# Kernel optimization log

Hardware: AMD Instinct MI355X
Metric: run time of the kernel (lower is better)

Reference implementation:

```python
import jax, jax.numpy as jnp
import numpy as np
import math

EMB = 512
HEADS = 8
FM = 56
WS = 7


def _relative_position_index(ws):
    coords = np.stack(np.meshgrid(np.arange(ws), np.arange(ws), indexing='ij')).reshape(2, -1)
    rel = coords[:, :, None] - coords[:, None, :]            # [2, ws^2, ws^2]
    rel = rel.transpose(1, 2, 0)                              # [ws^2, ws^2, 2]
    rel = rel + np.abs(rel.min())                             # shift to >= 0 (adds ws-1)
    rel[:, :, 0] = rel[:, :, 0] * (2 * ws - 1)
    return rel.sum(-1)                                        # [ws^2, ws^2] int

REL_IDX = jnp.asarray(_relative_position_index(WS))


def setup_inputs() -> dict:
    key = jax.random.key(0)
    ks = jax.random.split(key, 8)
    B, L, E = 16, FM * FM, EMB
    scale = 0.02
    return {
        'x': jax.random.normal(ks[0], (B, L, E), dtype=jnp.float32),
        'q_w': jax.random.normal(ks[1], (E, E), dtype=jnp.float32) * scale,
        'q_b': jax.random.normal(ks[2], (E,), dtype=jnp.float32) * scale,
        'k_w': jax.random.normal(ks[3], (E, E), dtype=jnp.float32) * scale,
        'k_b': jax.random.normal(ks[4], (E,), dtype=jnp.float32) * scale,
        'v_w': jax.random.normal(ks[5], (E, E), dtype=jnp.float32) * scale,
        'v_b': jax.random.normal(ks[6], (E,), dtype=jnp.float32) * scale,
        'bias_table': jax.random.normal(ks[7], ((2 * WS - 1) ** 2, HEADS), dtype=jnp.float32) * scale,
    }


def reference(x, q_w, q_b, k_w, k_b, v_w, v_b, bias_table):
    B, L, E = x.shape
    nh, d, ws = HEADS, E // HEADS, WS
    n = ws * ws
    # Faithful to the torch code: reshape (NOT channels-last transpose), then window partition
    xr = x.reshape(B, E, FM, FM)
    w = xr.reshape(B, FM // ws, ws, FM // ws, ws, E)
    w = jnp.transpose(w, (0, 1, 3, 2, 4, 5)).reshape(B, -1, ws, ws, E)  # [B, nW, ws, ws, E]
    nW = w.shape[1]
    # Linear projections (torch Linear: x @ W.T + b)
    q = (w @ q_w.T + q_b).reshape(B, nW, nh, n, d)
    k = (w @ k_w.T + k_b).reshape(B, nW, nh, n, d)
    v = (w @ v_w.T + v_b).reshape(B, nW, nh, n, d)
    # Relative position bias: [nh, n, n]
    bias = bias_table[REL_IDX.reshape(-1)].reshape(n, n, nh).transpose(2, 0, 1)
    scores = jnp.einsum('bwhqd,bwhkd->bwhqk', q, k) / math.sqrt(d)
    scores = scores + bias[None, None]
    attn = jax.nn.softmax(scores, axis=-1)
    out = jnp.einsum('bwhqk,bwhkd->bwhqd', attn, v)
    return out.reshape(B, L, E)
```

## Files before the change

kernel.cpp:

```cpp
#include <hip/hip_runtime.h>

typedef __attribute__((ext_vector_type(8))) short short8;
typedef __attribute__((ext_vector_type(4))) short short4v;
typedef __attribute__((ext_vector_type(4))) float float4v;
typedef __attribute__((ext_vector_type(8))) __bf16 bf16x8;

#define LDS_PQ 57344
#define LDS_PK 107520
#define LDS_TOTAL 157696

__device__ __forceinline__ unsigned short f2bf(float f) {
  unsigned u = __float_as_uint(f);
  u += 0x7FFFu + ((u >> 16) & 1u);
  return (unsigned short)(u >> 16);
}

__device__ __forceinline__ int pswz(int s) { return ((s ^ (s >> 3)) & 7) << 4; }

__global__ void wconv_kernel(const float* __restrict__ qw, const float* __restrict__ kw,
                             const float* __restrict__ vw, short* __restrict__ out) {
  int idx = blockIdx.x * 256 + threadIdx.x;
  int g = idx >> 15;
  int rem = idx & 32767;
  int lane = rem & 63;
  int n01 = (rem >> 6) & 1;
  int w   = (rem >> 7) & 15;
  int kk  = rem >> 11;
  int o  = w * 32 + n01 * 16 + (lane & 15);
  int k0 = kk * 32 + (lane >> 4) * 8;
  const float* src = (g == 0) ? qw : (g == 1) ? kw : vw;
  const float* p = src + o * 512 + k0;
  float4v v0 = *(const float4v*)(p);
  float4v v1 = *(const float4v*)(p + 4);
  short8 o8;
  o8[0] = (short)f2bf(v0.x); o8[1] = (short)f2bf(v0.y);
  o8[2] = (short)f2bf(v0.z); o8[3] = (short)f2bf(v0.w);
  o8[4] = (short)f2bf(v1.x); o8[5] = (short)f2bf(v1.y);
  o8[6] = (short)f2bf(v1.z); o8[7] = (short)f2bf(v1.w);
  *(short8*)(out + idx * 8) = o8;
}

__global__ void bexp_kernel(const float* __restrict__ btab, float* __restrict__ bexp) {
  int idx = blockIdx.x * 256 + threadIdx.x;
  float v = 0.f;
  if (idx < 21952) {
    int h = idx / 2744;
    int rem = idx - h * 2744;
    int i = rem / 56;
    int j = rem - i * 56;
    if (j < 49) {
      int yi = (i * 37) >> 8, xi = i - yi * 7;
      int yj = (j * 37) >> 8, xj = j - yj * 7;
      int t = (yi - yj + 6) * 13 + (xi - xj + 6);
      v = btab[t * 8 + h];
    }
  }
  bexp[idx] = v;
}

__global__ __launch_bounds__(1024, 4) void wattn_kernel(
    const float* __restrict__ x, const short* __restrict__ wcvt,
    const float* __restrict__ qb, const float* __restrict__ kb, const float* __restrict__ vb,
    const float* __restrict__ bexp, float* __restrict__ out) {
  __shared__ __align__(16) char sm[LDS_TOTAL];
  const int tid  = threadIdx.x;
  const int lane = tid & 63;
  const int wave = tid >> 6;
  const int bwi  = blockIdx.x;
  const int bb   = bwi >> 6, wi = bwi & 63;
  const int l15  = lane & 15;
  const int l4   = lane >> 4;
  const int ig   = l4 * 4;

  {
    const float* xb = x + (size_t)bb * (3136 * 512);
    const int whi = (wi >> 3) * 7, wlo = (wi & 7) * 7;
    for (int idx = tid; idx < 49 * 128; idx += 1024) {
      int t = idx >> 7, c4 = idx & 127;
      int yt = (t * 37) >> 8, xt = t - yt * 7;
      int l = (whi + yt) * 56 + wlo + xt;
      float4v v = *(const float4v*)(xb + l * 512 + c4 * 4);
      short4v o;
      o.x = (short)f2bf(v.x); o.y = (short)f2bf(v.y);
      o.z = (short)f2bf(v.z); o.w = (short)f2bf(v.w);
      int byte = t * 1024 + c4 * 8;
      *(short4v*)(sm + (byte ^ ((t & 7) << 4))) = o;
    }
  }
  __syncthreads();

  const int wcol = wave * 32;
  const int ckof = l4 * 16;

  int xbase[4], xsw[4];
#pragma unroll
  for (int mt = 0; mt < 4; ++mt) {
    int row = mt * 16 + l15;
    xbase[mt] = row * 1024;
    xsw[mt]   = (row & 7) << 4;
  }

  const short* wgb0 = wcvt + wave * 1024 + lane * 8;

#define LDWP(P, OFF) __builtin_bit_cast(bf16x8, *(const short8*)((P) + (OFF)))
#define LDX(MT, C) __builtin_bit_cast(bf16x8, *(const short8*)(sm + xbase[MT] + ((C) ^ xsw[MT])))

  {
    const short* wq = wgb0;
    const short* wk = wgb0 + 262144;
    float4v aq[2][4], ak[2][4];
#pragma unroll
    for (int nt = 0; nt < 2; ++nt)
#pragma unroll
      for (int mt = 0; mt < 4; ++mt) { aq[nt][mt] = (float4v)0.f; ak[nt][mt] = (float4v)0.f; }

    bf16x8 uq0 = LDWP(wq, 0), uq1 = LDWP(wq, 512);
    bf16x8 uk0 = LDWP(wk, 0), uk1 = LDWP(wk, 512);

#pragma unroll 1
    for (int kk = 0; kk < 16; ++kk) {
      const int nko = ((kk + 1) & 15) * 16384;
      bf16x8 nq0 = LDWP(wq, nko), nq1 = LDWP(wq, nko + 512);
      bf16x8 nk0 = LDWP(wk, nko), nk1 = LDWP(wk, nko + 512);
      const int c_ = kk * 64 + ckof;
      bf16x8 x0 = LDX(0, c_), x1 = LDX(1, c_), x2 = LDX(2, c_), x3 = LDX(3, c_);
      __builtin_amdgcn_s_setprio(1);
      aq[0][0] = __builtin_amdgcn_mfma_f32_16x16x32_bf16(uq0, x0, aq[0][0], 0, 0, 0);
      aq[1][0] = __builtin_amdgcn_mfma_f32_16x16x32_bf16(uq1, x0, aq[1][0], 0, 0, 0);
      ak[0][0] = __builtin_amdgcn_mfma_f32_16x16x32_bf16(uk0, x0, ak[0][0], 0, 0, 0);
      ak[1][0] = __builtin_amdgcn_mfma_f32_16x16x32_bf16(uk1, x0, ak[1][0], 0, 0, 0);
      aq[0][1] = __builtin_amdgcn_mfma_f32_16x16x32_bf16(uq0, x1, aq[0][1], 0, 0, 0);
      aq[1][1] = __builtin_amdgcn_mfma_f32_16x16x32_bf16(uq1, x1, aq[1][1], 0, 0, 0);
      ak[0][1] = __builtin_amdgcn_mfma_f32_16x16x32_bf16(uk0, x1, ak[0][1], 0, 0, 0);
      ak[1][1] = __builtin_amdgcn_mfma_f32_16x16x32_bf16(uk1, x1, ak[1][1], 0, 0, 0);
      aq[0][2] = __builtin_amdgcn_mfma_f32_16x16x32_bf16(uq0, x2, aq[0][2], 0, 0, 0);
      aq[1][2] = __builtin_amdgcn_mfma_f32_16x16x32_bf16(uq1, x2, aq[1][2], 0, 0, 0);
      ak[0][2] = __builtin_amdgcn_mfma_f32_16x16x32_bf16(uk0, x2, ak[0][2], 0, 0, 0);
      ak[1][2] = __builtin_amdgcn_mfma_f32_16x16x32_bf16(uk1, x2, ak[1][2], 0, 0, 0);
      aq[0][3] = __builtin_amdgcn_mfma_f32_16x16x32_bf16(uq0, x3, aq[0][3], 0, 0, 0);
      aq[1][3] = __builtin_amdgcn_mfma_f32_16x16x32_bf16(uq1, x3, aq[1][3], 0, 0, 0);
      ak[0][3] = __builtin_amdgcn_mfma_f32_16x16x32_bf16(uk0, x3, ak[0][3], 0, 0, 0);
      ak[1][3] = __builtin_amdgcn_mfma_f32_16x16x32_bf16(uk1, x3, ak[1][3], 0, 0, 0);
      __builtin_amdgcn_s_setprio(0);
      uq0 = nq0; uq1 = nq1; uk0 = nk0; uk1 = nk1;
    }

#pragma unroll
    for (int nt = 0; nt < 2; ++nt) {
      int o0 = wcol + nt * 16 + ig;
      float4v bq = *(const float4v*)(qb + o0);
      float4v bk = *(const float4v*)(kb + o0);
      int dd0 = o0 & 63, sg = o0 >> 6;
#pragma unroll
      for (int mt = 0; mt < 4; ++mt) {
        int t = mt * 16 + l15;
        if (t < 49) {
          int s = t * 8 + sg;
          int addr = (s * 128 + dd0 * 2) ^ pswz(s);
          short4v pq, pk;
#pragma unroll
          for (int r = 0; r < 4; ++r) {
            pq[r] = (short)f2bf((aq[nt][mt][r] + bq[r]) * 0.125f);
            pk[r] = (short)f2bf(ak[nt][mt][r] + bk[r]);
          }
          *(short4v*)(sm + LDS_PQ + addr) = pq;
          *(short4v*)(sm + LDS_PK + addr) = pk;
        }
      }
    }
  }

  {
    const short* wgb = wgb0 + 2 * 262144;
    float4v acc[2][4];
#pragma unroll
    for (int nt = 0; nt < 2; ++nt)
#pragma unroll
      for (int mt = 0; mt < 4; ++mt) acc[nt][mt] = (float4v)0.f;

    bf16x8 wa0 = LDWP(wgb, 0),     wa1 = LDWP(wgb, 512);
    bf16x8 wb0 = LDWP(wgb, 16384), wb1 = LDWP(wgb, 16384 + 512);
    bf16x8 wc0, wc1, wd0, wd1;

#define GEMM_PHASE(KIDX, W0, W1)                                                          \
    do {                                                                                  \
      const int c_ = (KIDX) * 64 + ckof;                                                  \
      bf16x8 x0_ = LDX(0, c_), x1_ = LDX(1, c_), x2_ = LDX(2, c_), x3_ = LDX(3, c_);      \
      __builtin_amdgcn_s_setprio(1);                                                      \
      acc[0][0] = __builtin_amdgcn_mfma_f32_16x16x32_bf16(W0, x0_, acc[0][0], 0, 0, 0);   \
      acc[1][0] = __builtin_amdgcn_mfma_f32_16x16x32_bf16(W1, x0_, acc[1][0], 0, 0, 0);   \
      acc[0][1] = __builtin_amdgcn_mfma_f32_16x16x32_bf16(W0, x1_, acc[0][1], 0, 0, 0);   \
      acc[1][1] = __builtin_amdgcn_mfma_f32_16x16x32_bf16(W1, x1_, acc[1][1], 0, 0, 0);   \
      acc[0][2] = __builtin_amdgcn_mfma_f32_16x16x32_bf16(W0, x2_, acc[0][2], 0, 0, 0);   \
      acc[1][2] = __builtin_amdgcn_mfma_f32_16x16x32_bf16(W1, x2_, acc[1][2], 0, 0, 0);   \
      acc[0][3] = __builtin_amdgcn_mfma_f32_16x16x32_bf16(W0, x3_, acc[0][3], 0, 0, 0);   \
      acc[1][3] = __builtin_amdgcn_mfma_f32_16x16x32_bf16(W1, x3_, acc[1][3], 0, 0, 0);   \
      __builtin_amdgcn_s_setprio(0);                                                      \
    } while (0)

#pragma unroll 1
    for (int kk = 0; kk < 16; kk += 4) {
      wc0 = LDWP(wgb, ((kk + 2) & 15) * 16384); wc1 = LDWP(wgb, ((kk + 2) & 15) * 16384 + 512);
      GEMM_PHASE(kk, wa0, wa1);
      wd0 = LDWP(wgb, ((kk + 3) & 15) * 16384); wd1 = LDWP(wgb, ((kk + 3) & 15) * 16384 + 512);
      GEMM_PHASE(kk + 1, wb0, wb1);
      wa0 = LDWP(wgb, ((kk + 4) & 15) * 16384); wa1 = LDWP(wgb, ((kk + 4) & 15) * 16384 + 512);
      GEMM_PHASE(kk + 2, wc0, wc1);
      wb0 = LDWP(wgb, ((kk + 5) & 15) * 16384); wb1 = LDWP(wgb, ((kk + 5) & 15) * 16384 + 512);
      GEMM_PHASE(kk + 3, wd0, wd1);
    }
#undef GEMM_PHASE

    __syncthreads();
#pragma unroll
    for (int nt = 0; nt < 2; ++nt) {
      int o0 = wcol + nt * 16 + ig;
      float4v bv = *(const float4v*)(vb + o0);
      int dd0 = o0 & 63, sg = o0 >> 6;
#pragma unroll
      for (int mt = 0; mt < 4; ++mt) {
        int t = mt * 16 + l15;
        if (t < 49) {
          int s = t * 8 + sg;
          int h2 = (s * 1339) >> 16;
          int colb = h2 * 112 + (s - h2 * 49) * 2;
#pragma unroll
          for (int r = 0; r < 4; ++r) {
            int dd = dd0 + r;
            *(unsigned short*)(sm + ((dd * 896 + colb) ^ ((dd & 7) << 4))) =
                f2bf(acc[nt][mt][r] + bv[r]);
          }
        }
      }
    }
    if (tid < 512) {
      int h2 = tid >> 6, dd = tid & 63;
      int rowb = dd * 896 + h2 * 112;
      int swz = (dd & 7) << 4;
#pragma unroll
      for (int q = 49; q < 56; ++q)
        *(unsigned short*)(sm + ((rowb + q * 2) ^ swz)) = 0;
    }
  }

  const int h  = wave & 7;
  const int mh = wave >> 3;

  float4v sc[4][2];
#pragma unroll
  for (int jt = 0; jt < 4; ++jt)
#pragma unroll
    for (int it = 0; it < 2; ++it) sc[jt][it] = (float4v)0.f;

#pragma unroll
  for (int ks = 0; ks < 2; ++ks) {
    const int dd = ks * 32 + l4 * 8;
    bf16x8 kf[4], qf[2];
#pragma unroll
    for (int jt = 0; jt < 4; ++jt) {
      int s = h * 49 + jt * 16 + l15;
      int flat = s * 128 + dd * 2;
      kf[jt] = __builtin_bit_cast(bf16x8, *(const short8*)(sm + LDS_PK + (flat ^ pswz(s))));
    }
#pragma unroll
    for (int it = 0; it < 2; ++it) {
      int s = h * 49 + (mh * 2 + it) * 16 + l15;
      int flat = s * 128 + dd * 2;
      qf[it] = __builtin_bit_cast(bf16x8, *(const short8*)(sm + LDS_PQ + (flat ^ pswz(s))));
    }
    __builtin_amdgcn_s_setprio(1);
#pragma unroll
    for (int jt = 0; jt < 4; ++jt)
#pragma unroll
      for (int it = 0; it < 2; ++it)
        sc[jt][it] = __builtin_amdgcn_mfma_f32_16x16x32_bf16(kf[jt], qf[it], sc[jt][it], 0, 0, 0);
    __builtin_amdgcn_s_setprio(0);
  }

  const float* bx = bexp + h * 2744;
#pragma unroll
  for (int it = 0; it < 2; ++it) {
    int i = (mh * 2 + it) * 16 + l15;
    const float* bi = bx + ((i > 48) ? 48 : i) * 56 + ig;
    float mx = -1e30f;
#pragma unroll
    for (int jt = 0; jt < 4; ++jt) {
      float4v b4 = *(const float4v*)(bi + jt * 16);
#pragma unroll
      for (int r = 0; r < 4; ++r) {
        int j = jt * 16 + ig + r;
        float v = (i < 49 && j < 49) ? sc[jt][it][r] + b4[r] : -1e30f;
        sc[jt][it][r] = v;
        mx = fmaxf(mx, v);
      }
    }
    mx = fmaxf(mx, __shfl_xor(mx, 16));
    mx = fmaxf(mx, __shfl_xor(mx, 32));
    float ssum = 0.f;
#pragma unroll
    for (int jt = 0; jt < 4; ++jt)
#pragma unroll
      for (int r = 0; r < 4; ++r) {
        float e = __expf(sc[jt][it][r] - mx);
        sc[jt][it][r] = e;
        ssum += e;
      }
    ssum += __shfl_xor(ssum, 16);
    ssum += __shfl_xor(ssum, 32);
    float inv = 1.f / ssum;
#pragma unroll
    for (int jt = 0; jt < 4; ++jt)
#pragma unroll
      for (int r = 0; r < 4; ++r) sc[jt][it][r] *= inv;
  }

#pragma unroll
  for (int it = 0; it < 2; ++it) {
    int i = (mh * 2 + it) * 16 + l15;
    if (i < 49) {
      int s = h * 49 + i;
      int rowb = s * 128;
      int swz = pswz(s);
#pragma unroll
      for (int jt = 0; jt < 4; ++jt) {
        short4v pk;
#pragma unroll
        for (int r = 0; r < 4; ++r) pk[r] = (short)f2bf(sc[jt][it][r]);
        *(short4v*)(sm + LDS_PQ + ((rowb + jt * 32 + ig * 2) ^ swz)) = pk;
      }
    }
  }

  __syncthreads();

  float4v oacc[4][2];
#pragma unroll
  for (int dt = 0; dt < 4; ++dt)
#pragma unroll
    for (int tt = 0; tt < 2; ++tt) oacc[dt][tt] = (float4v)0.f;

#pragma unroll
  for (int ks = 0; ks < 2; ++ks) {
    const int tp0 = ks * 32 + l4 * 8;
    bf16x8 vf[4], af[2];
#pragma unroll
    for (int dt = 0; dt < 4; ++dt) {
      int dd = dt * 16 + l15;
      vf[dt] = __builtin_bit_cast(bf16x8,
          *(const short8*)(sm + ((dd * 896 + h * 112 + tp0 * 2) ^ ((dd & 7) << 4))));
    }
#pragma unroll
    for (int tt = 0; tt < 2; ++tt) {
      int t = (mh * 2 + tt) * 16 + l15;
      int tr = (t > 48) ? 48 : t;
      int s = h * 49 + tr;
      af[tt] = __builtin_bit_cast(bf16x8,
          *(const short8*)(sm + LDS_PQ + ((s * 128 + tp0 * 2) ^ pswz(s))));
    }
    __builtin_amdgcn_s_setprio(1);
#pragma unroll
    for (int dt = 0; dt < 4; ++dt)
#pragma unroll
      for (int tt = 0; tt < 2; ++tt)
        oacc[dt][tt] = __builtin_amdgcn_mfma_f32_16x16x32_bf16(vf[dt], af[tt], oacc[dt][tt], 0, 0, 0);
    __builtin_amdgcn_s_setprio(0);
  }

  float* op = out + (size_t)bwi * 25088 + h * 3136;
#pragma unroll
  for (int tt = 0; tt < 2; ++tt) {
    int t = (mh * 2 + tt) * 16 + l15;
    if (t < 49) {
#pragma unroll
      for (int dt = 0; dt < 4; ++dt)
        *(float4v*)(op + t * 64 + dt * 16 + ig) = oacc[dt][tt];
    }
  }
#undef LDWP
#undef LDX
}

extern "C" void kernel_launch(void* const* d_in, const int* in_sizes, int n_in,
                              void* d_out, int out_size, void* d_ws, size_t ws_size,
                              hipStream_t stream) {
  const float* x    = (const float*)d_in[0];
  const float* q_w  = (const float*)d_in[1];
  const float* q_b  = (const float*)d_in[2];
  const float* k_w  = (const float*)d_in[3];
  const float* k_b  = (const float*)d_in[4];
  const float* v_w  = (const float*)d_in[5];
  const float* v_b  = (const float*)d_in[6];
  const float* btab = (const float*)d_in[7];
  short* wcvt = (short*)d_ws;
  float* bexp = (float*)((char*)d_ws + 3 * 262144 * 2);

  hipLaunchKernelGGL(wconv_kernel, dim3(384), dim3(256), 0, stream, q_w, k_w, v_w, wcvt);
  hipLaunchKernelGGL(bexp_kernel, dim3(86), dim3(256), 0, stream, btab, bexp);
  hipLaunchKernelGGL(wattn_kernel, dim3(1024), dim3(1024), 0, stream,
                     x, wcvt, q_b, k_b, v_b, bexp, (float*)d_out);
}
```

Before: 149.4 us.

## Make attention kernel persistent over windows, fold q scale into weights, use packed bf16 converts

The main kernel now launches 256 blocks that each loop over four windows, instead of one block per window for 1024 blocks. A barrier at the top of each iteration protects shared-memory reuse. The 1/sqrt(d) query scale moves into the weight-conversion pre-kernel and the bias, and f32-to-bf16 rounding now uses the hardware v_cvt_pk_bf16_f32 instruction instead of integer bit manipulation. The goal is less block launch and tail overhead and fewer ALU ops, at the risk of lower parallelism, since 256 blocks with roughly 154 KB of LDS each may leave some CUs idle, with no overlap of load and compute across iterations.

Measured after the change: 241.3 us. +61.5%, slower.

```diff
diff --git a/kernel.cpp b/kernel.cpp
--- a/kernel.cpp
+++ b/kernel.cpp
@@ -3,6 +3,7 @@
 typedef __attribute__((ext_vector_type(8))) short short8;
 typedef __attribute__((ext_vector_type(4))) short short4v;
 typedef __attribute__((ext_vector_type(4))) float float4v;
+typedef __attribute__((ext_vector_type(2))) unsigned int uint2v;
 typedef __attribute__((ext_vector_type(8))) __bf16 bf16x8;
 
 #define LDS_PQ 57344
@@ -13,6 +14,12 @@
   unsigned u = __float_as_uint(f);
   u += 0x7FFFu + ((u >> 16) & 1u);
   return (unsigned short)(u >> 16);
+}
+
+__device__ __forceinline__ unsigned cvtpk(float lo, float hi) {
+  unsigned r;
+  asm("v_cvt_pk_bf16_f32 %0, %1, %2" : "=v"(r) : "v"(lo), "v"(hi));
+  return r;
 }
 
 __device__ __forceinline__ int pswz(int s) { return ((s ^ (s >> 3)) & 7) << 4; }
@@ -29,14 +36,15 @@
   int o  = w * 32 + n01 * 16 + (lane & 15);
   int k0 = kk * 32 + (lane >> 4) * 8;
   const float* src = (g == 0) ? qw : (g == 1) ? kw : vw;
+  const float sc = (g == 0) ? 0.125f : 1.0f;
   const float* p = src + o * 512 + k0;
   float4v v0 = *(const float4v*)(p);
   float4v v1 = *(const float4v*)(p + 4);
   short8 o8;
-  o8[0] = (short)f2bf(v0.x); o8[1] = (short)f2bf(v0.y);
-  o8[2] = (short)f2bf(v0.z); o8[3] = (short)f2bf(v0.w);
-  o8[4] = (short)f2bf(v1.x); o8[5] = (short)f2bf(v1.y);
-  o8[6] = (short)f2bf(v1.z); o8[7] = (short)f2bf(v1.w);
+  o8[0] = (short)f2bf(v0.x * sc); o8[1] = (short)f2bf(v0.y * sc);
+  o8[2] = (short)f2bf(v0.z * sc); o8[3] = (short)f2bf(v0.w * sc);
+  o8[4] = (short)f2bf(v1.x * sc); o8[5] = (short)f2bf(v1.y * sc);
+  o8[6] = (short)f2bf(v1.z * sc); o8[7] = (short)f2bf(v1.w * sc);
   *(short8*)(out + idx * 8) = o8;
 }
 
@@ -66,31 +74,13 @@
   const int tid  = threadIdx.x;
   const int lane = tid & 63;
   const int wave = tid >> 6;
-  const int bwi  = blockIdx.x;
-  const int bb   = bwi >> 6, wi = bwi & 63;
   const int l15  = lane & 15;
   const int l4   = lane >> 4;
   const int ig   = l4 * 4;
-
-  {
-    const float* xb = x + (size_t)bb * (3136 * 512);
-    const int whi = (wi >> 3) * 7, wlo = (wi & 7) * 7;
-    for (int idx = tid; idx < 49 * 128; idx += 1024) {
-      int t = idx >> 7, c4 = idx & 127;
-      int yt = (t * 37) >> 8, xt = t - yt * 7;
-      int l = (whi + yt) * 56 + wlo + xt;
-      float4v v = *(const float4v*)(xb + l * 512 + c4 * 4);
-      short4v o;
-      o.x = (short)f2bf(v.x); o.y = (short)f2bf(v.y);
-      o.z = (short)f2bf(v.z); o.w = (short)f2bf(v.w);
-      int byte = t * 1024 + c4 * 8;
-      *(short4v*)(sm + (byte ^ ((t & 7) << 4))) = o;
-    }
-  }
-  __syncthreads();
-
   const int wcol = wave * 32;
   const int ckof = l4 * 16;
+  const int h    = wave & 7;
+  const int mh   = wave >> 3;
 
   int xbase[4], xsw[4];
 #pragma unroll
@@ -105,275 +95,297 @@
 #define LDWP(P, OFF) __builtin_bit_cast(bf16x8, *(const short8*)((P) + (OFF)))
 #define LDX(MT, C) __builtin_bit_cast(bf16x8, *(const short8*)(sm + xbase[MT] + ((C) ^ xsw[MT])))
 
-  {
-    const short* wq = wgb0;
-    const short* wk = wgb0 + 262144;
-    float4v aq[2][4], ak[2][4];
-#pragma unroll
-    for (int nt = 0; nt < 2; ++nt)
-#pragma unroll
-      for (int mt = 0; mt < 4; ++mt) { aq[nt][mt] = (float4v)0.f; ak[nt][mt] = (float4v)0.f; }
-
-    bf16x8 uq0 = LDWP(wq, 0), uq1 = LDWP(wq, 512);
-    bf16x8 uk0 = LDWP(wk, 0), uk1 = LDWP(wk, 512);
-
 #pragma unroll 1
-    for (int kk = 0; kk < 16; ++kk) {
-      const int nko = ((kk + 1) & 15) * 16384;
-      bf16x8 nq0 = LDWP(wq, nko), nq1 = LDWP(wq, nko + 512);
-      bf16x8 nk0 = LDWP(wk, nko), nk1 = LDWP(wk, nko + 512);
-      const int c_ = kk * 64 + ckof;
-      bf16x8 x0 = LDX(0, c_), x1 = LDX(1, c_), x2 = LDX(2, c_), x3 = LDX(3, c_);
-      __builtin_amdgcn_s_setprio(1);
-      aq[0][0] = __builtin_amdgcn_mfma_f32_16x16x32_bf16(uq0, x0, aq[0][0], 0, 0, 0);
-      aq[1][0] = __builtin_amdgcn_mfma_f32_16x16x32_bf16(uq1, x0, aq[1][0], 0, 0, 0);
-      ak[0][0] = __builtin_amdgcn_mfma_f32_16x16x32_bf16(uk0, x0, ak[0][0], 0, 0, 0);
-      ak[1][0] = __builtin_amdgcn_mfma_f32_16x16x32_bf16(uk1, x0, ak[1][0], 0, 0, 0);
-      aq[0][1] = __builtin_amdgcn_mfma_f32_16x16x32_bf16(uq0, x1, aq[0][1], 0, 0, 0);
-      aq[1][1] = __builtin_amdgcn_mfma_f32_16x16x32_bf16(uq1, x1, aq[1][1], 0, 0, 0);
-      ak[0][1] = __builtin_amdgcn_mfma_f32_16x16x32_bf16(uk0, x1, ak[0][1], 0, 0, 0);
-      ak[1][1] = __builtin_amdgcn_mfma_f32_16x16x32_bf16(uk1, x1, ak[1][1], 0, 0, 0);
-      aq[0][2] = __builtin_amdgcn_mfma_f32_16x16x32_bf16(uq0, x2, aq[0][2], 0, 0, 0);
-      aq[1][2] = __builtin_amdgcn_mfma_f32_16x16x32_bf16(uq1, x2, aq[1][2], 0, 0, 0);
-      ak[0][2] = __builtin_amdgcn_mfma_f32_16x16x32_bf16(uk0, x2, ak[0][2], 0, 0, 0);
-      ak[1][2] = __builtin_amdgcn_mfma_f32_16x16x32_bf16(uk1, x2, ak[1][2], 0, 0, 0);
-      aq[0][3] = __builtin_amdgcn_mfma_f32_16x16x32_bf16(uq0, x3, aq[0][3], 0, 0, 0);
-      aq[1][3] = __builtin_amdgcn_mfma_f32_16x16x32_bf16(uq1, x3, aq[1][3], 0, 0, 0);
-      ak[0][3] = __builtin_amdgcn_mfma_f32_16x16x32_bf16(uk0, x3, ak[0][3], 0, 0, 0);
-      ak[1][3] = __builtin_amdgcn_mfma_f32_16x16x32_bf16(uk1, x3, ak[1][3], 0, 0, 0);
-      __builtin_amdgcn_s_setprio(0);
-      uq0 = nq0; uq1 = nq1; uk0 = nk0; uk1 = nk1;
-    }
-
-#pragma unroll
-    for (int nt = 0; nt < 2; ++nt) {
-      int o0 = wcol + nt * 16 + ig;
-      float4v bq = *(const float4v*)(qb + o0);
-      float4v bk = *(const float4v*)(kb + o0);
-      int dd0 = o0 & 63, sg = o0 >> 6;
-#pragma unroll
-      for (int mt = 0; mt < 4; ++mt) {
-        int t = mt * 16 + l15;
-        if (t < 49) {
-          int s = t * 8 + sg;
-          int addr = (s * 128 + dd0 * 2) ^ pswz(s);
-          short4v pq, pk;
-#pragma unroll
-          for (int r = 0; r < 4; ++r) {
-            pq[r] = (short)f2bf((aq[nt][mt][r] + bq[r]) * 0.125f);
-            pk[r] = (short)f2bf(ak[nt][mt][r] + bk[r]);
-          }
-          *(short4v*)(sm + LDS_PQ + addr) = pq;
-          *(short4v*)(sm + LDS_PK + addr) = pk;
-        }
-      }
-    }
-  }
-
-  {
-    const short* wgb = wgb0 + 2 * 262144;
-    float4v acc[2][4];
-#pragma unroll
-    for (int nt = 0; nt < 2; ++nt)
-#pragma unroll
-      for (int mt = 0; mt < 4; ++mt) acc[nt][mt] = (float4v)0.f;
-
-    bf16x8 wa0 = LDWP(wgb, 0),     wa1 = LDWP(wgb, 512);
-    bf16x8 wb0 = LDWP(wgb, 16384), wb1 = LDWP(wgb, 16384 + 512);
-    bf16x8 wc0, wc1, wd0, wd1;
-
-#define GEMM_PHASE(KIDX, W0, W1)                                                          \
-    do {                                                                                  \
-      const int c_ = (KIDX) * 64 + ckof;                                                  \
-      bf16x8 x0_ = LDX(0, c_), x1_ = LDX(1, c_), x2_ = LDX(2, c_), x3_ = LDX(3, c_);      \
-      __builtin_amdgcn_s_setprio(1);                                                      \
-      acc[0][0] = __builtin_amdgcn_mfma_f32_16x16x32_bf16(W0, x0_, acc[0][0], 0, 0, 0);   \
-      acc[1][0] = __builtin_amdgcn_mfma_f32_16x16x32_bf16(W1, x0_, acc[1][0], 0, 0, 0);   \
-      acc[0][1] = __builtin_amdgcn_mfma_f32_16x16x32_bf16(W0, x1_, acc[0][1], 0, 0, 0);   \
-      acc[1][1] = __builtin_amdgcn_mfma_f32_16x16x32_bf16(W1, x1_, acc[1][1], 0, 0, 0);   \
-      acc[0][2] = __builtin_amdgcn_mfma_f32_16x16x32_bf16(W0, x2_, acc[0][2], 0, 0, 0);   \
-      acc[1][2] = __builtin_amdgcn_mfma_f32_16x16x32_bf16(W1, x2_, acc[1][2], 0, 0, 0);   \
-      acc[0][3] = __builtin_amdgcn_mfma_f32_16x16x32_bf16(W0, x3_, acc[0][3], 0, 0, 0);   \
-      acc[1][3] = __builtin_amdgcn_mfma_f32_16x16x32_bf16(W1, x3_, acc[1][3], 0, 0, 0);   \
-      __builtin_amdgcn_s_setprio(0);                                                      \
-    } while (0)
+  for (int bwi = blockIdx.x; bwi < 1024; bwi += 256) {
+    const int bb = bwi >> 6, wi = bwi & 63;
+
+    __syncthreads();
+
+    {
+      const float* xb = x + (size_t)bb * (3136 * 512);
+      const int whi = (wi >> 3) * 7, wlo = (wi & 7) * 7;
+      for (int idx = tid; idx < 49 * 128; idx += 1024) {
+        int t = idx >> 7, c4 = idx & 127;
+        int yt = (t * 37) >> 8, xt = t - yt * 7;
+        int l = (whi + yt) * 56 + wlo + xt;
+        float4v v = *(const float4v*)(xb + l * 512 + c4 * 4);
+        uint2v o;
+        o.x = cvtpk(v.x, v.y);
+        o.y = cvtpk(v.z, v.w);
+        int byte = t * 1024 + c4 * 8;
+        *(uint2v*)(sm + (byte ^ ((t & 7) << 4))) = o;
+      }
+    }
+    __syncthreads();
+
+    {
+      const short* wq = wgb0;
+      const short* wk = wgb0 + 262144;
+      float4v aq[2][4], ak[2][4];
+#pragma unroll
+      for (int nt = 0; nt < 2; ++nt)
+#pragma unroll
+        for (int mt = 0; mt < 4; ++mt) { aq[nt][mt] = (float4v)0.f; ak[nt][mt] = (float4v)0.f; }
+
+      bf16x8 uq0 = LDWP(wq, 0), uq1 = LDWP(wq, 512);
+      bf16x8 uk0 = LDWP(wk, 0), uk1 = LDWP(wk, 512);
 
 #pragma unroll 1
-    for (int kk = 0; kk < 16; kk += 4) {
-      wc0 = LDWP(wgb, ((kk + 2) & 15) * 16384); wc1 = LDWP(wgb, ((kk + 2) & 15) * 16384 + 512);
-      GEMM_PHASE(kk, wa0, wa1);
-      wd0 = LDWP(wgb, ((kk + 3) & 15) * 16384); wd1 = LDWP(wgb, ((kk + 3) & 15) * 16384 + 512);
-      GEMM_PHASE(kk + 1, wb0, wb1);
-      wa0 = LDWP(wgb, ((kk + 4) & 15) * 16384); wa1 = LDWP(wgb, ((kk + 4) & 15) * 16384 + 512);
-      GEMM_PHASE(kk + 2, wc0, wc1);
-      wb0 = LDWP(wgb, ((kk + 5) & 15) * 16384); wb1 = LDWP(wgb, ((kk + 5) & 15) * 16384 + 512);
-      GEMM_PHASE(kk + 3, wd0, wd1);
-    }
-#undef GEMM_PHASE
-
-    __syncthreads();
-#pragma unroll
-    for (int nt = 0; nt < 2; ++nt) {
-      int o0 = wcol + nt * 16 + ig;
-      float4v bv = *(const float4v*)(vb + o0);
-      int dd0 = o0 & 63, sg = o0 >> 6;
-#pragma unroll
-      for (int mt = 0; mt < 4; ++mt) {
-        int t = mt * 16 + l15;
-        if (t < 49) {
-          int s = t * 8 + sg;
-          int h2 = (s * 1339) >> 16;
-          int colb = h2 * 112 + (s - h2 * 49) * 2;
-#pragma unroll
-          for (int r = 0; r < 4; ++r) {
-            int dd = dd0 + r;
-            *(unsigned short*)(sm + ((dd * 896 + colb) ^ ((dd & 7) << 4))) =
-                f2bf(acc[nt][mt][r] + bv[r]);
+      for (int kk = 0; kk < 16; ++kk) {
+        const int nko = ((kk + 1) & 15) * 16384;
+        bf16x8 nq0 = LDWP(wq, nko), nq1 = LDWP(wq, nko + 512);
+        bf16x8 nk0 = LDWP(wk, nko), nk1 = LDWP(wk, nko + 512);
+        const int c_ = kk * 64 + ckof;
+        bf16x8 x0 = LDX(0, c_), x1 = LDX(1, c_), x2 = LDX(2, c_), x3 = LDX(3, c_);
+        __builtin_amdgcn_s_setprio(1);
+        aq[0][0] = __builtin_amdgcn_mfma_f32_16x16x32_bf16(uq0, x0, aq[0][0], 0, 0, 0);
+        aq[1][0] = __builtin_amdgcn_mfma_f32_16x16x32_bf16(uq1, x0, aq[1][0], 0, 0, 0);
+        ak[0][0] = __builtin_amdgcn_mfma_f32_16x16x32_bf16(uk0, x0, ak[0][0], 0, 0, 0);
+        ak[1][0] = __builtin_amdgcn_mfma_f32_16x16x32_bf16(uk1, x0, ak[1][0], 0, 0, 0);
+        aq[0][1] = __builtin_amdgcn_mfma_f32_16x16x32_bf16(uq0, x1, aq[0][1], 0, 0, 0);
+        aq[1][1] = __builtin_amdgcn_mfma_f32_16x16x32_bf16(uq1, x1, aq[1][1], 0, 0, 0);
+        ak[0][1] = __builtin_amdgcn_mfma_f32_16x16x32_bf16(uk0, x1, ak[0][1], 0, 0, 0);
+        ak[1][1] = __builtin_amdgcn_mfma_f32_16x16x32_bf16(uk1, x1, ak[1][1], 0, 0, 0);
+        aq[0][2] = __builtin_amdgcn_mfma_f32_16x16x32_bf16(uq0, x2, aq[0][2], 0, 0, 0);
+        aq[1][2] = __builtin_amdgcn_mfma_f32_16x16x32_bf16(uq1, x2, aq[1][2], 0, 0, 0);
+        ak[0][2] = __builtin_amdgcn_mfma_f32_16x16x32_bf16(uk0, x2, ak[0][2], 0, 0, 0);
+        ak[1][2] = __builtin_amdgcn_mfma_f32_16x16x32_bf16(uk1, x2, ak[1][2], 0, 0, 0);
+        aq[0][3] = __builtin_amdgcn_mfma_f32_16x16x32_bf16(uq0, x3, aq[0][3], 0, 0, 0);
+        aq[1][3] = __builtin_amdgcn_mfma_f32_16x16x32_bf16(uq1, x3, aq[1][3], 0, 0, 0);
+        ak[0][3] = __builtin_amdgcn_mfma_f32_16x16x32_bf16(uk0, x3, ak[0][3], 0, 0, 0);
+        ak[1][3] = __builtin_amdgcn_mfma_f32_16x16x32_bf16(uk1, x3, ak[1][3], 0, 0, 0);
+        __builtin_amdgcn_s_setprio(0);
+        uq0 = nq0; uq1 = nq1; uk0 = nk0; uk1 = nk1;
+      }
+
+#pragma unroll
+      for (int nt = 0; nt < 2; ++nt) {
+        int o0 = wcol + nt * 16 + ig;
+        float4v bq = *(const float4v*)(qb + o0);
+        float4v bk = *(const float4v*)(kb + o0);
+#pragma unroll
+        for (int r = 0; r < 4; ++r) bq[r] *= 0.125f;
+        int dd0 = o0 & 63, sg = o0 >> 6;
+#pragma unroll
+        for (int mt = 0; mt < 4; ++mt) {
+          int t = mt * 16 + l15;
+          if (t < 49) {
+            int s = t * 8 + sg;
+            int addr = (s * 128 + dd0 * 2) ^ pswz(s);
+            uint2v pq, pk;
+            pq.x = cvtpk(aq[nt][mt][0] + bq[0], aq[nt][mt][1] + bq[1]);
+            pq.y = cvtpk(aq[nt][mt][2] + bq[2], aq[nt][mt][3] + bq[3]);
+            pk.x = cvtpk(ak[nt][mt][0] + bk[0], ak[nt][mt][1] + bk[1]);
+            pk.y = cvtpk(ak[nt][mt][2] + bk[2], ak[nt][mt][3] + bk[3]);
+            *(uint2v*)(sm + LDS_PQ + addr) = pq;
+            *(uint2v*)(sm + LDS_PK + addr) = pk;
           }
         }
       }
     }
-    if (tid < 512) {
-      int h2 = tid >> 6, dd = tid & 63;
-      int rowb = dd * 896 + h2 * 112;
-      int swz = (dd & 7) << 4;
-#pragma unroll
-      for (int q = 49; q < 56; ++q)
-        *(unsigned short*)(sm + ((rowb + q * 2) ^ swz)) = 0;
-    }
-  }
-
-  const int h  = wave & 7;
-  const int mh = wave >> 3;
-
-  float4v sc[4][2];
-#pragma unroll
-  for (int jt = 0; jt < 4; ++jt)
-#pragma unroll
-    for (int it = 0; it < 2; ++it) sc[jt][it] = (float4v)0.f;
-
-#pragma unroll
-  for (int ks = 0; ks < 2; ++ks) {
-    const int dd = ks * 32 + l4 * 8;
-    bf16x8 kf[4], qf[2];
-#pragma unroll
-    for (int jt = 0; jt < 4; ++jt) {
-      int s = h * 49 + jt * 16 + l15;
-      int flat = s * 128 + dd * 2;
-      kf[jt] = __builtin_bit_cast(bf16x8, *(const short8*)(sm + LDS_PK + (flat ^ pswz(s))));
-    }
+
+    {
+      const short* wgb = wgb0 + 2 * 262144;
+      float4v acc[2][4];
+#pragma unroll
+      for (int nt = 0; nt < 2; ++nt)
+#pragma unroll
+        for (int mt = 0; mt < 4; ++mt) acc[nt][mt] = (float4v)0.f;
+
+      bf16x8 wa0 = LDWP(wgb, 0),     wa1 = LDWP(wgb, 512);
+      bf16x8 wb0 = LDWP(wgb, 16384), wb1 = LDWP(wgb, 16384 + 512);
+      bf16x8 wc0, wc1, wd0, wd1;
+
+#define GEMM_PHASE(KIDX, W0, W1)                                                          \
+      do {                                                                                \
+        const int c_ = (KIDX) * 64 + ckof;                                                \
+        bf16x8 x0_ = LDX(0, c_), x1_ = LDX(1, c_), x2_ = LDX(2, c_), x3_ = LDX(3, c_);    \
+        __builtin_amdgcn_s_setprio(1);                                                    \
+        acc[0][0] = __builtin_amdgcn_mfma_f32_16x16x32_bf16(W0, x0_, acc[0][0], 0, 0, 0); \
+        acc[1][0] = __builtin_amdgcn_mfma_f32_16x16x32_bf16(W1, x0_, acc[1][0], 0, 0, 0); \
+        acc[0][1] = __builtin_amdgcn_mfma_f32_16x16x32_bf16(W0, x1_, acc[0][1], 0, 0, 0); \
+        acc[1][1] = __builtin_amdgcn_mfma_f32_16x16x32_bf16(W1, x1_, acc[1][1], 0, 0, 0); \
+        acc[0][2] = __builtin_amdgcn_mfma_f32_16x16x32_bf16(W0, x2_, acc[0][2], 0, 0, 0); \
+        acc[1][2] = __builtin_amdgcn_mfma_f32_16x16x32_bf16(W1, x2_, acc[1][2], 0, 0, 0); \
+        acc[0][3] = __builtin_amdgcn_mfma_f32_16x16x32_bf16(W0, x3_, acc[0][3], 0, 0, 0); \
+        acc[1][3] = __builtin_amdgcn_mfma_f32_16x16x32_bf16(W1, x3_, acc[1][3], 0, 0, 0); \
+        __builtin_amdgcn_s_setprio(0);                                                    \
+      } while (0)
+
+#pragma unroll 1
+      for (int kk = 0; kk < 16; kk += 4) {
+        wc0 = LDWP(wgb, ((kk + 2) & 15) * 16384); wc1 = LDWP(wgb, ((kk + 2) & 15) * 16384 + 512);
+        GEMM_PHASE(kk, wa0, wa1);
+        wd0 = LDWP(wgb, ((kk + 3) & 15) * 16384); wd1 = LDWP(wgb, ((kk + 3) & 15) * 16384 + 512);
+        GEMM_PHASE(kk + 1, wb0, wb1);
+        wa0 = LDWP(wgb, ((kk + 4) & 15) * 16384); wa1 = LDWP(wgb, ((kk + 4) & 15) * 16384 + 512);
+        GEMM_PHASE(kk + 2, wc0, wc1);
+        wb0 = LDWP(wgb, ((kk + 5) & 15) * 16384); wb1 = LDWP(wgb, ((kk + 5) & 15) * 16384 + 512);
+        GEMM_PHASE(kk + 3, wd0, wd1);
+      }
+#undef GEMM_PHASE
+
+      __syncthreads();
+#pragma unroll
+      for (int nt = 0; nt < 2; ++nt) {
+        int o0 = wcol + nt * 16 + ig;
+        float4v bv = *(const float4v*)(vb + o0);
+        int dd0 = o0 & 63, sg = o0 >> 6;
+#pragma unroll
+        for (int mt = 0; mt < 4; ++mt) {
+          int t = mt * 16 + l15;
+          if (t < 49) {
+            int s = t * 8 + sg;
+            int h2 = (s * 1339) >> 16;
+            int colb = h2 * 112 + (s - h2 * 49) * 2;
+#pragma unroll
+            for (int r = 0; r < 4; ++r) {
+              int dd = dd0 + r;
+              *(unsigned short*)(sm + ((dd * 896 + colb) ^ ((dd & 7) << 4))) =
+                  f2bf(acc[nt][mt][r] + bv[r]);
+            }
+          }
+        }
+      }
+      if (tid < 512) {
+        int h2 = tid >> 6, dd = tid & 63;
+        int rowb = dd * 896 + h2 * 112;
+        int swz = (dd & 7) << 4;
+#pragma unroll
+        for (int q = 49; q < 56; ++q)
+          *(unsigned short*)(sm + ((rowb + q * 2) ^ swz)) = 0;
+      }
+    }
+
+    float4v sc[4][2];
+#pragma unroll
+    for (int jt = 0; jt < 4; ++jt)
+#pragma unroll
+      for (int it = 0; it < 2; ++it) sc[jt][it] = (float4v)0.f;
+
+#pragma unroll
+    for (int ks = 0; ks < 2; ++ks) {
+      const int dd = ks * 32 + l4 * 8;
+      bf16x8 kf[4], qf[2];
+#pragma unroll
+      for (int jt = 0; jt < 4; ++jt) {
+        int s = h * 49 + jt * 16 + l15;
+        int flat = s * 128 + dd * 2;
+        kf[jt] = __builtin_bit_cast(bf16x8, *(const short8*)(sm + LDS_PK + (flat ^ pswz(s))));
+      }
+#pragma unroll
+      for (int it = 0; it < 2; ++it) {
+        int s = h * 49 + (mh * 2 + it) * 16 + l15;
+        int flat = s * 128 + dd * 2;
+        qf[it] = __builtin_bit_cast(bf16x8, *(const short8*)(sm + LDS_PQ + (flat ^ pswz(s))));
+      }
+      __builtin_amdgcn_s_setprio(1);
+#pragma unroll
+      for (int jt = 0; jt < 4; ++jt)
+#pragma unroll
+        for (int it = 0; it < 2; ++it)
+          sc[jt][it] = __builtin_amdgcn_mfma_f32_16x16x32_bf16(kf[jt], qf[it], sc[jt][it], 0, 0, 0);
+      __builtin_amdgcn_s_setprio(0);
+    }
+
+    const float* bx = bexp + h * 2744;
 #pragma unroll
     for (int it = 0; it < 2; ++it) {
-      int s = h * 49 + (mh * 2 + it) * 16 + l15;
-      int flat = s * 128 + dd * 2;
-      qf[it] = __builtin_bit_cast(bf16x8, *(const short8*)(sm + LDS_PQ + (flat ^ pswz(s))));
-    }
-    __builtin_amdgcn_s_setprio(1);
-#pragma unroll
-    for (int jt = 0; jt < 4; ++jt)
-#pragma unroll
-      for (int it = 0; it < 2; ++it)
-        sc[jt][it] = __builtin_amdgcn_mfma_f32_16x16x32_bf16(kf[jt], qf[it], sc[jt][it], 0, 0, 0);
-    __builtin_amdgcn_s_setprio(0);
-  }
-
-  const float* bx = bexp + h * 2744;
-#pragma unroll
-  for (int it = 0; it < 2; ++it) {
-    int i = (mh * 2 + it) * 16 + l15;
-    const float* bi = bx + ((i > 48) ? 48 : i) * 56 + ig;
-    float mx = -1e30f;
-#pragma unroll
-    for (int jt = 0; jt < 4; ++jt) {
-      float4v b4 = *(const float4v*)(bi + jt * 16);
-#pragma unroll
-      for (int r = 0; r < 4; ++r) {
-        int j = jt * 16 + ig + r;
-        float v = (i < 49 && j < 49) ? sc[jt][it][r] + b4[r] : -1e30f;
-        sc[jt][it][r] = v;
-        mx = fmaxf(mx, v);
-      }
-    }
-    mx = fmaxf(mx, __shfl_xor(mx, 16));
-    mx = fmaxf(mx, __shfl_xor(mx, 32));
-    float ssum = 0.f;
-#pragma unroll
-    for (int jt = 0; jt < 4; ++jt)
-#pragma unroll
-      for (int r = 0; r < 4; ++r) {
-        float e = __expf(sc[jt][it][r] - mx);
-        sc[jt][it][r] = e;
-        ssum += e;
-      }
-    ssum += __shfl_xor(ssum, 16);
-    ssum += __shfl_xor(ssum, 32);
-    float inv = 1.f / ssum;
-#pragma unroll
-    for (int jt = 0; jt < 4; ++jt)
-#pragma unroll
-      for (int r = 0; r < 4; ++r) sc[jt][it][r] *= inv;
-  }
-
-#pragma unroll
-  for (int it = 0; it < 2; ++it) {
-    int i = (mh * 2 + it) * 16 + l15;
-    if (i < 49) {
-      int s = h * 49 + i;
-      int rowb = s * 128;
-      int swz = pswz(s);
+      int i = (mh * 2 + it) * 16 + l15;
+      const float* bi = bx + ((i > 48) ? 48 : i) * 56 + ig;
+      float mx = -1e30f;
 #pragma unroll
       for (int jt = 0; jt < 4; ++jt) {
-        short4v pk;
-#pragma unroll
-        for (int r = 0; r < 4; ++r) pk[r] = (short)f2bf(sc[jt][it][r]);
-        *(short4v*)(sm + LDS_PQ + ((rowb + jt * 32 + ig * 2) ^ swz)) = pk;
-      }
-    }
-  }
-
-  __syncthreads();
-
-  float4v oacc[4][2];
-#pragma unroll
-  for (int dt = 0; dt < 4; ++dt)
-#pragma unroll
-    for (int tt = 0; tt < 2; ++tt) oacc[dt][tt] = (float4v)0.f;
-
-#pragma unroll
-  for (int ks = 0; ks < 2; ++ks) {
-    const int tp0 = ks * 32 + l4 * 8;
-    bf16x8 vf[4], af[2];
-#pragma unroll
-    for (int dt = 0; dt < 4; ++dt) {
-      int dd = dt * 16 + l15;
-      vf[dt] = __builtin_bit_cast(bf16x8,
-          *(const short8*)(sm + ((dd * 896 + h * 112 + tp0 * 2) ^ ((dd & 7) << 4))));
-    }
+        float4v b4 = *(const float4v*)(bi + jt * 16);
+#pragma unroll
+        for (int r = 0; r < 4; ++r) {
+          int j = jt * 16 + ig + r;
+          float v = (i < 49 && j < 49) ? sc[jt][it][r] + b4[r] : -1e30f;
+          sc[jt][it][r] = v;
+          mx = fmaxf(mx, v);
+        }
+      }
+      mx = fmaxf(mx, __shfl_xor(mx, 16));
+      mx = fmaxf(mx, __shfl_xor(mx, 32));
+      float ssum = 0.f;
+#pragma unroll
+      for (int jt = 0; jt < 4; ++jt)
+#pragma unroll
+        for (int r = 0; r < 4; ++r) {
+          float e = __expf(sc[jt][it][r] - mx);
+          sc[jt][it][r] = e;
+          ssum += e;
+        }
+      ssum += __shfl_xor(ssum, 16);
+      ssum += __shfl_xor(ssum, 32);
+      float inv = 1.f / ssum;
+#pragma unroll
+      for (int jt = 0; jt < 4; ++jt)
+#pragma unroll
+        for (int r = 0; r < 4; ++r) sc[jt][it][r] *= inv;
+    }
+
+#pragma unroll
+    for (int it = 0; it < 2; ++it) {
+      int i = (mh * 2 + it) * 16 + l15;
+      if (i < 49) {
+        int s = h * 49 + i;
+        int rowb = s * 128;
+        int swz = pswz(s);
+#pragma unroll
+        for (int jt = 0; jt < 4; ++jt) {
+          uint2v pk2;
+          pk2.x = cvtpk(sc[jt][it][0], sc[jt][it][1]);
+          pk2.y = cvtpk(sc[jt][it][2], sc[jt][it][3]);
+          *(uint2v*)(sm + LDS_PQ + ((rowb + jt * 32 + ig * 2) ^ swz)) = pk2;
+        }
+      }
+    }
+
+    __syncthreads();
+
+    float4v oacc[4][2];
+#pragma unroll
+    for (int dt = 0; dt < 4; ++dt)
+#pragma unroll
+      for (int tt = 0; tt < 2; ++tt) oacc[dt][tt] = (float4v)0.f;
+
+#pragma unroll
+    for (int ks = 0; ks < 2; ++ks) {
+      const int tp0 = ks * 32 + l4 * 8;
+      bf16x8 vf[4], af[2];
+#pragma unroll
+      for (int dt = 0; dt < 4; ++dt) {
+        int dd = dt * 16 + l15;
+        vf[dt] = __builtin_bit_cast(bf16x8,
+            *(const short8*)(sm + ((dd * 896 + h * 112 + tp0 * 2) ^ ((dd & 7) << 4))));
+      }
+#pragma unroll
+      for (int tt = 0; tt < 2; ++tt) {
+        int t = (mh * 2 + tt) * 16 + l15;
+        int tr = (t > 48) ? 48 : t;
+        int s = h * 49 + tr;
+        af[tt] = __builtin_bit_cast(bf16x8,
+            *(const short8*)(sm + LDS_PQ + ((s * 128 + tp0 * 2) ^ pswz(s))));
+      }
+      __builtin_amdgcn_s_setprio(1);
+#pragma unroll
+      for (int dt = 0; dt < 4; ++dt)
+#pragma unroll
+        for (int tt = 0; tt < 2; ++tt)
+          oacc[dt][tt] = __builtin_amdgcn_mfma_f32_16x16x32_bf16(vf[dt], af[tt], oacc[dt][tt], 0, 0, 0);
+      __builtin_amdgcn_s_setprio(0);
+    }
+
+    float* op = out + (size_t)bwi * 25088 + h * 3136;
 #pragma unroll
     for (int tt = 0; tt < 2; ++tt) {
       int t = (mh * 2 + tt) * 16 + l15;
-      int tr = (t > 48) ? 48 : t;
-      int s = h * 49 + tr;
-      af[tt] = __builtin_bit_cast(bf16x8,
-          *(const short8*)(sm + LDS_PQ + ((s * 128 + tp0 * 2) ^ pswz(s))));
-    }
-    __builtin_amdgcn_s_setprio(1);
-#pragma unroll
-    for (int dt = 0; dt < 4; ++dt)
-#pragma unroll
-      for (int tt = 0; tt < 2; ++tt)
-        oacc[dt][tt] = __builtin_amdgcn_mfma_f32_16x16x32_bf16(vf[dt], af[tt], oacc[dt][tt], 0, 0, 0);
-    __builtin_amdgcn_s_setprio(0);
-  }
-
-  float* op = out + (size_t)bwi * 25088 + h * 3136;
-#pragma unroll
-  for (int tt = 0; tt < 2; ++tt) {
-    int t = (mh * 2 + tt) * 16 + l15;
-    if (t < 49) {
-#pragma unroll
-      for (int dt = 0; dt < 4; ++dt)
-        *(float4v*)(op + t * 64 + dt * 16 + ig) = oacc[dt][tt];
+      if (t < 49) {
+#pragma unroll
+        for (int dt = 0; dt < 4; ++dt)
+          *(float4v*)(op + t * 64 + dt * 16 + ig) = oacc[dt][tt];
+      }
     }
   }
 #undef LDWP
@@ -396,6 +408,6 @@
 
   hipLaunchKernelGGL(wconv_kernel, dim3(384), dim3(256), 0, stream, q_w, k_w, v_w, wcvt);
   hipLaunchKernelGGL(bexp_kernel, dim3(86), dim3(256), 0, stream, btab, bexp);
-  hipLaunchKernelGGL(wattn_kernel, dim3(1024), dim3(1024), 0, stream,
+  hipLaunchKernelGGL(wattn_kernel, dim3(256), dim3(1024), 0, stream,
                      x, wcvt, q_b, k_b, v_b, bexp, (float*)d_out);
 }
```
